# Kernel optimization log

Measured on AMD Instinct MI355X. Metric: run time of the kernel, lower is better.

Reference implementation:

```python
import jax, jax.numpy as jnp
import numpy as np

N, IN_DIM, E, EDGE_DIM = 50000, 128, 600000, 16
D, H, L = 128, 4, 2
C = D // H  # 32
NEG_SLOPE = 0.2
EPS = 1e-5


def setup_inputs() -> dict:
    key = jax.random.key(0)
    ks = jax.random.split(key, 20)
    x = jax.random.normal(ks[0], (N, IN_DIM), dtype=jnp.float32)
    src = jax.random.randint(ks[1], (E,), 0, N)
    dst = jax.random.randint(ks[2], (E,), 0, N)
    src = jnp.where(src == dst, (src + 1) % N, src)  # no pre-existing self loops
    edge_index = jnp.stack([src, dst]).astype(jnp.int64)
    edge_attr = jax.random.normal(ks[3], (E, EDGE_DIM), dtype=jnp.float32)
    s = 0.05
    p = {
        'in_w': jax.random.normal(ks[4], (IN_DIM, D)) * s,
        'in_b': jnp.zeros((D,), jnp.float32),
        'Wl': jax.random.normal(ks[5], (L, D, D)) * s,
        'bl': jnp.zeros((L, D), jnp.float32),
        'Wr': jax.random.normal(ks[6], (L, D, D)) * s,
        'br': jnp.zeros((L, D), jnp.float32),
        'We': jax.random.normal(ks[7], (L, EDGE_DIM, D)) * s,
        'att': jax.random.normal(ks[8], (L, H, C)) * s,
        'cb': jnp.zeros((L, D), jnp.float32),
        'ln_g': jnp.ones((D,), jnp.float32),
        'ln_b': jnp.zeros((D,), jnp.float32),
        'h1w': jax.random.normal(ks[9], (D, D // 2)) * s,
        'h1b': jnp.zeros((D // 2,), jnp.float32),
        'h2w': jax.random.normal(ks[10], (D // 2, 3)) * s,
        'h2b': jnp.zeros((3,), jnp.float32),
    }
    return {'x': x, 'edge_index': edge_index, 'edge_attr': edge_attr, **p}


def _forward(x, edge_attr, in_w, in_b, Wl, bl, Wr, br, We, att, cb,
             ln_g, ln_b, h1w, h1b, h2w, h2b, src0, dst0):
    n = x.shape[0]
    # add_self_loops with fill_value='mean': loop edge_attr = mean of incoming edge_attr per node
    deg = jax.ops.segment_sum(jnp.ones_like(dst0, dtype=x.dtype), dst0, n)
    loop_attr = jax.ops.segment_sum(edge_attr, dst0, n) / jnp.maximum(deg, 1.0)[:, None]
    idx = jnp.arange(n, dtype=src0.dtype)
    src = jnp.concatenate([src0, idx])
    dst = jnp.concatenate([dst0, idx])
    ea = jnp.concatenate([edge_attr, loop_attr])  # [E+N, EDGE_DIM]

    h = x @ in_w + in_b  # [N, D]
    for l in range(L):
        xl = (h @ Wl[l] + bl[l]).reshape(n, H, C)
        xr = (h @ Wr[l] + br[l]).reshape(n, H, C)
        ee = (ea @ We[l]).reshape(-1, H, C)
        m = xl[src] + xr[dst] + ee                      # [E', H, C]
        m = jnp.where(m > 0, m, NEG_SLOPE * m)          # LeakyReLU(0.2)
        logit = jnp.einsum('ehc,hc->eh', m, att[l])     # [E', H]
        mx = jax.ops.segment_max(logit, dst, n)         # every node has a self loop -> finite
        a = jnp.exp(logit - mx[dst])
        den = jax.ops.segment_sum(a, dst, n)
        a = a / den[dst]                                # scatter softmax over destinations
        out = jax.ops.segment_sum(a[..., None] * xl[src], dst, n)  # [N, H, C]
        h = jax.nn.elu(out.reshape(n, D) + cb[l])       # conv bias then ELU (dropout=eval)
    mu = jnp.mean(h, axis=-1, keepdims=True)
    var = jnp.mean((h - mu) ** 2, axis=-1, keepdims=True)
    h = (h - mu) * jax.lax.rsqrt(var + EPS) * ln_g + ln_b
    h = jax.nn.relu(h @ h1w + h1b)
    return h @ h2w + h2b  # [N, 3]


def reference(x, edge_index, edge_attr, in_w, in_b, Wl, bl, Wr, br, We, att, cb,
              ln_g, ln_b, h1w, h1b, h2w, h2b):
    return _forward(x, edge_attr, in_w, in_b, Wl, bl, Wr, br, We, att, cb,
                    ln_g, ln_b, h1w, h1b, h2w, h2b, edge_index[0], edge_index[1])
```

## Files before the change

### kernel.cpp

```cpp
#include <hip/hip_runtime.h>

#define NEG_SLOPE 0.2f
#define LN_EPS 1e-5f

typedef float f2 __attribute__((ext_vector_type(2)));
typedef short s16x4 __attribute__((ext_vector_type(4)));
typedef short s16x8 __attribute__((ext_vector_type(8)));
typedef float f32x4 __attribute__((ext_vector_type(4)));
typedef unsigned au32 __attribute__((may_alias));

__device__ __forceinline__ f2 sp2(float x){ return (f2){x, x}; }
__device__ __forceinline__ f2 fma2(f2 a, f2 b, f2 c){
#if __has_builtin(__builtin_elementwise_fma)
  return __builtin_elementwise_fma(a, b, c);
#else
  f2 r; r.x = fmaf(a.x, b.x, c.x); r.y = fmaf(a.y, b.y, c.y); return r;
#endif
}
__device__ __forceinline__ f2 max2(f2 a, f2 b){
#if __has_builtin(__builtin_elementwise_max)
  return __builtin_elementwise_max(a, b);
#else
  f2 r; r.x = fmaxf(a.x, b.x); r.y = fmaxf(a.y, b.y); return r;
#endif
}
__device__ __forceinline__ f2 min2(f2 a, f2 b){
#if __has_builtin(__builtin_elementwise_min)
  return __builtin_elementwise_min(a, b);
#else
  f2 r; r.x = fminf(a.x, b.x); r.y = fminf(a.y, b.y); return r;
#endif
}
__device__ __forceinline__ float wsum64(float v){
  #pragma unroll
  for (int o = 32; o >= 1; o >>= 1) v += __shfl_xor(v, o);
  return v;
}
__device__ __forceinline__ unsigned short f2b(float f){
  unsigned u = __float_as_uint(f);
  return (unsigned short)((u + 0x7fffu + ((u >> 16) & 1u)) >> 16);
}

__global__ void k_count(const int* __restrict__ dst, int* __restrict__ deg, int E){
  int e = blockIdx.x * blockDim.x + threadIdx.x;
  if (e < E) atomicAdd(&deg[dst[e]], 1);
}

__global__ void k_scan_blk(const int* __restrict__ deg, int* __restrict__ part,
                           int* __restrict__ sums, int n){
  __shared__ int buf[256];
  int t = threadIdx.x, i = blockIdx.x * 256 + t;
  int v = (i < n) ? deg[i] : 0;
  buf[t] = v; __syncthreads();
  #pragma unroll
  for (int off = 1; off < 256; off <<= 1){
    int x = (t >= off) ? buf[t - off] : 0;
    __syncthreads(); buf[t] += x; __syncthreads();
  }
  if (i < n) part[i] = buf[t] - v;
  if (t == 255) sums[blockIdx.x] = buf[255];
}

__global__ void k_scan_top(int* __restrict__ sums, int nb){
  __shared__ int buf[256];
  int t = threadIdx.x;
  int v = (t < nb) ? sums[t] : 0;
  buf[t] = v; __syncthreads();
  #pragma unroll
  for (int off = 1; off < 256; off <<= 1){
    int x = (t >= off) ? buf[t - off] : 0;
    __syncthreads(); buf[t] += x; __syncthreads();
  }
  if (t < nb) sums[t] = buf[t] - v;
}

__global__ void k_scan_add(int* __restrict__ ptr, const int* __restrict__ sums,
                           int n, int Etot){
  int i = blockIdx.x * 256 + threadIdx.x;
  if (i < n) ptr[i] += sums[blockIdx.x];
  if (i == 0) ptr[n] = Etot;
}

__global__ void k_fill(const int* __restrict__ dst, const int* __restrict__ src,
                       int* __restrict__ cnt, const int* __restrict__ ptr,
                       const float* __restrict__ ea, unsigned short* __restrict__ ceab,
                       int* __restrict__ sx, int E){
  int e = blockIdx.x * blockDim.x + threadIdx.x;
  if (e < E){
    int d = dst[e];
    int pos = atomicAdd(&cnt[d], 1);
    int p = ptr[d] + pos;
    sx[p] = src[e];
    const float4* s4 = (const float4*)(ea + (size_t)e * 16);
    float4 a0 = s4[0], a1 = s4[1], a2 = s4[2], a3 = s4[3];
    ushort4 o0 = {f2b(a0.x), f2b(a0.y), f2b(a0.z), f2b(a0.w)};
    ushort4 o1 = {f2b(a1.x), f2b(a1.y), f2b(a1.z), f2b(a1.w)};
    ushort4 o2 = {f2b(a2.x), f2b(a2.y), f2b(a2.z), f2b(a2.w)};
    ushort4 o3 = {f2b(a3.x), f2b(a3.y), f2b(a3.z), f2b(a3.w)};
    ushort4* d4 = (ushort4*)(ceab + (size_t)p * 16);
    d4[0] = o0; d4[1] = o1; d4[2] = o2; d4[3] = o3;
  }
}

__global__ void k_cvt(const float* __restrict__ X, unsigned short* __restrict__ Xb,
                      long n4){
  long i = (long)blockIdx.x * blockDim.x + threadIdx.x;
  long i4 = i * 4;
  if (i4 < n4){
    float4 v = *(const float4*)(X + i4);
    ushort4 o; o.x = f2b(v.x); o.y = f2b(v.y); o.z = f2b(v.z); o.w = f2b(v.w);
    *(ushort4*)(Xb + i4) = o;
  }
}

__global__ void k_pack(const float* __restrict__ w0, const float* __restrict__ w1,
                       const float* __restrict__ w2, const float* __restrict__ w3,
                       const float* __restrict__ w4, unsigned short* __restrict__ Bp){
  int id = blockIdx.x * blockDim.x + threadIdx.x;
  if (id >= 5 * 2048) return;
  int mat = id >> 11, rem = id & 2047;
  int c = rem >> 8, q = (rem >> 6) & 3, l = rem & 63;
  const float* W = mat == 0 ? w0 : mat == 1 ? w1 : mat == 2 ? w2 : mat == 3 ? w3 : w4;
  unsigned short* o = Bp + ((size_t)mat * 2048 + rem) * 8;
  int kb = q * 32 + (l >> 4) * 8;
  int col = c * 16 + (l & 15);
  #pragma unroll
  for (int j = 0; j < 8; j++) o[j] = f2b(W[(kb + j) * 128 + col]);
}

__global__ void k_packwe(const float* __restrict__ We, unsigned short* __restrict__ Bpwe){
  int id = blockIdx.x * blockDim.x + threadIdx.x;
  if (id >= 2 * 8 * 64) return;
  int layer = id >> 9, rem = id & 511, c = rem >> 6, l = rem & 63;
  const float* W = We + (size_t)layer * 2048;
  unsigned short* o = Bpwe + (size_t)id * 8;
  int kb = (l >> 4) * 8;
  int col = c * 16 + (l & 15);
  #pragma unroll
  for (int j = 0; j < 8; j++){
    int k = kb + j;
    o[j] = (k < 16) ? f2b(W[k * 128 + col]) : (unsigned short)0;
  }
}

__launch_bounds__(256)
__global__ void k_mm(const unsigned short* __restrict__ A,
                     const unsigned short* __restrict__ Bp,
                     const float* __restrict__ bias,
                     unsigned short* __restrict__ Yb, int M){
  const int ln = threadIdx.x & 63;
  const int rowBase = (blockIdx.x * 4 + (threadIdx.x >> 6)) * 16;
  const int r16 = ln & 15, quad = ln >> 4;
  int row = rowBase + r16; if (row >= M) row = M - 1;
  const unsigned short* ap = A + (size_t)row * 128 + quad * 8;
  s16x8 af[4];
  #pragma unroll
  for (int q = 0; q < 4; q++) af[q] = *(const s16x8*)(ap + q * 32);
  f32x4 acc[8];
  #pragma unroll
  for (int c = 0; c < 8; c++){
    acc[c] = (f32x4){0.f, 0.f, 0.f, 0.f};
    #pragma unroll
    for (int q = 0; q < 4; q++){
      s16x8 bf = *(const s16x8*)(Bp + ((size_t)(c * 4 + q) * 64 + ln) * 8);
      acc[c] = __builtin_amdgcn_mfma_f32_16x16x32_bf16(af[q], bf, acc[c], 0, 0, 0);
    }
  }
  #pragma unroll
  for (int c = 0; c < 8; c++){
    int col = c * 16 + r16;
    float bv = bias[col];
    #pragma unroll
    for (int r = 0; r < 4; r++){
      int orow = rowBase + quad * 4 + r;
      if (orow < M) Yb[(size_t)orow * 128 + col] = f2b(acc[c][r] + bv);
    }
  }
}

__launch_bounds__(256)
__global__ void k_mm_lr(const unsigned short* __restrict__ A,
                        const unsigned short* __restrict__ BpL,
                        const unsigned short* __restrict__ BpR,
                        const float* __restrict__ bL, const float* __restrict__ bR,
                        float* __restrict__ YL, float* __restrict__ YR, int M){
  const int ln = threadIdx.x & 63;
  const int rowBase = (blockIdx.x * 4 + (threadIdx.x >> 6)) * 16;
  const int r16 = ln & 15, quad = ln >> 4;
  int row = rowBase + r16; if (row >= M) row = M - 1;
  const unsigned short* ap = A + (size_t)row * 128 + quad * 8;
  s16x8 af[4];
  #pragma unroll
  for (int q = 0; q < 4; q++) af[q] = *(const s16x8*)(ap + q * 32);
  f32x4 aL[8], aR[8];
  #pragma unroll
  for (int c = 0; c < 8; c++){
    aL[c] = (f32x4){0.f, 0.f, 0.f, 0.f};
    aR[c] = (f32x4){0.f, 0.f, 0.f, 0.f};
    #pragma unroll
    for (int q = 0; q < 4; q++){
      s16x8 bfl = *(const s16x8*)(BpL + ((size_t)(c * 4 + q) * 64 + ln) * 8);
      s16x8 bfr = *(const s16x8*)(BpR + ((size_t)(c * 4 + q) * 64 + ln) * 8);
      aL[c] = __builtin_amdgcn_mfma_f32_16x16x32_bf16(af[q], bfl, aL[c], 0, 0, 0);
      aR[c] = __builtin_amdgcn_mfma_f32_16x16x32_bf16(af[q], bfr, aR[c], 0, 0, 0);
    }
  }
  #pragma unroll
  for (int c = 0; c < 8; c++){
    int col = c * 16 + r16;
    float bvl = bL[col], bvr = bR[col];
    #pragma unroll
    for (int r = 0; r < 4; r++){
      int orow = rowBase + quad * 4 + r;
      if (orow < M){
        YL[(size_t)orow * 128 + col] = aL[c][r] + bvl;
        YR[(size_t)orow * 128 + col] = aR[c][r] + bvr;
      }
    }
  }
}

__launch_bounds__(256)
__global__ void k_gat(const float* __restrict__ xl, const float* __restrict__ xr,
                      const unsigned short* __restrict__ ceab,
                      const int* __restrict__ sx, const int* __restrict__ ptr,
                      const unsigned short* __restrict__ Bpwe,
                      const float* __restrict__ att, const float* __restrict__ cbv,
                      float* __restrict__ hf, unsigned short* __restrict__ hb,
                      int N, int wf, int wb){
  __shared__ unsigned short lee[4][16 * 130];
  const int t = threadIdx.x & 63;
  const int wv = threadIdx.x >> 6;
  const int c0 = 2 * t;
  const int l15 = t & 15, q = t >> 4;

  s16x8 bwe[8];
  #pragma unroll
  for (int c = 0; c < 8; c++) bwe[c] = *(const s16x8*)(Bpwe + ((size_t)c * 64 + t) * 8);
  const f2 atv = *(const f2*)(att + c0);
  const f2 cbf = *(const f2*)(cbv + c0);
  unsigned short* lw = &lee[wv][0];
  const int wbase = q * 4 * 130 + l15;

  for (int n = blockIdx.x * 4 + wv; n < N; n += gridDim.x * 4){
    const int beg = __builtin_amdgcn_readfirstlane(ptr[n]);
    const int end = __builtin_amdgcn_readfirstlane(ptr[n + 1]);
    const int deg = end - beg;

    const f2 xrv = *(const f2*)(xr + (size_t)n * 128 + c0);
    const f2 xln = *(const f2*)(xl + (size_t)n * 128 + c0);

    f2 acc = sp2(0.f), eesum = sp2(0.f);
    float den = 0.f;

    for (int cbase = beg; cbase < end; cbase += 64){
      const int cn = __builtin_amdgcn_readfirstlane(min(64, end - cbase));
      int sv = (t < cn) ? sx[cbase + t] : 0;

      for (int sub = 0; sub < cn; sub += 16){
        s16x8 af = (s16x8){0, 0, 0, 0, 0, 0, 0, 0};
        if (q < 2)
          af = *(const s16x8*)(ceab + (size_t)(cbase + sub + l15) * 16 + q * 8);
        f2 xs[16];
        #pragma unroll
        for (int i = 0; i < 16; i++){
          int s = __builtin_amdgcn_readlane(sv, sub + i);
          xs[i] = *(const f2*)(xl + (size_t)s * 128 + c0);
        }
        #pragma unroll
        for (int c = 0; c < 8; c++){
          f32x4 ee4 = __builtin_amdgcn_mfma_f32_16x16x32_bf16(
              af, bwe[c], (f32x4){0.f, 0.f, 0.f, 0.f}, 0, 0, 0);
          #pragma unroll
          for (int r = 0; r < 4; r++)
            lw[wbase + r * 130 + c * 16] = f2b(ee4[r]);
        }
        #pragma unroll
        for (int i = 0; i < 16; i++){
          const int item = sub + i;
          const float vm = (item < cn) ? 1.f : 0.f;
          const int it = (item < cn) ? i : 0;
          au32 pp = *(const au32*)&lw[it * 130 + c0];
          f2 ee;
          ee.x = __uint_as_float(pp << 16);
          ee.y = __uint_as_float(pp & 0xffff0000u);
          eesum = fma2(sp2(vm), ee, eesum);
          f2 m = xs[i] + xrv + ee;
          m = fma2(sp2(NEG_SLOPE), min2(m, sp2(0.f)), max2(m, sp2(0.f)));
          f2 pr = m * atv;
          float pl = pr.x + pr.y;
          pl += __shfl_xor(pl, 1); pl += __shfl_xor(pl, 2);
          pl += __shfl_xor(pl, 4); pl += __shfl_xor(pl, 8);
          float p = __expf(pl) * vm;
          den += p;
          acc = fma2(sp2(p), xs[i], acc);
        }
      }
    }

    {
      float rdeg = 1.f / fmaxf((float)deg, 1.f);
      f2 m = xln + xrv + eesum * sp2(rdeg);
      m = fma2(sp2(NEG_SLOPE), min2(m, sp2(0.f)), max2(m, sp2(0.f)));
      f2 pr = m * atv;
      float pl = pr.x + pr.y;
      pl += __shfl_xor(pl, 1); pl += __shfl_xor(pl, 2);
      pl += __shfl_xor(pl, 4); pl += __shfl_xor(pl, 8);
      float p = __expf(pl);
      den += p;
      acc = fma2(sp2(p), xln, acc);
    }

    float rd = 1.f / den;
    f2 o = fma2(acc, sp2(rd), cbf);
    float o0 = o.x > 0.f ? o.x : expm1f(o.x);
    float o1 = o.y > 0.f ? o.y : expm1f(o.y);
    if (wf) *(f2*)(hf + (size_t)n * 128 + c0) = (f2){o0, o1};
    if (wb){
      unsigned packed = (unsigned)f2b(o0) | ((unsigned)f2b(o1) << 16);
      *(unsigned*)(hb + (size_t)n * 128 + c0) = packed;
    }
  }
}

__launch_bounds__(256)
__global__ void k_head(const float* __restrict__ h, const float* __restrict__ g,
                       const float* __restrict__ b, const float* __restrict__ w1,
                       const float* __restrict__ b1, const float* __restrict__ w2,
                       const float* __restrict__ b2, float* __restrict__ out, int N){
  __shared__ float sn[4][128];
  const int t = threadIdx.x & 63, wv = threadIdx.x >> 6;
  for (int node = blockIdx.x * 4 + wv; node < N; node += gridDim.x * 4){
    float h0 = h[(size_t)node * 128 + t];
    float h1 = h[(size_t)node * 128 + 64 + t];
    float mu = wsum64(h0 + h1) * (1.f / 128.f);
    float d0 = h0 - mu, d1 = h1 - mu;
    float var = wsum64(d0 * d0 + d1 * d1) * (1.f / 128.f);
    float rstd = rsqrtf(var + LN_EPS);
    sn[wv][t]      = d0 * rstd * g[t]      + b[t];
    sn[wv][t + 64] = d1 * rstd * g[t + 64] + b[t + 64];
    float a = b1[t];
    #pragma unroll
    for (int k4 = 0; k4 < 32; k4++){
      float4 v = *(const float4*)&sn[wv][k4 * 4];
      a = fmaf(v.x, w1[(k4 * 4 + 0) * 64 + t], a);
      a = fmaf(v.y, w1[(k4 * 4 + 1) * 64 + t], a);
      a = fmaf(v.z, w1[(k4 * 4 + 2) * 64 + t], a);
      a = fmaf(v.w, w1[(k4 * 4 + 3) * 64 + t], a);
    }
    a = fmaxf(a, 0.f);
    float p0 = a * w2[t * 3 + 0], p1 = a * w2[t * 3 + 1], p2 = a * w2[t * 3 + 2];
    p0 = wsum64(p0); p1 = wsum64(p1); p2 = wsum64(p2);
    if (t == 0){
      out[(size_t)node * 3 + 0] = p0 + b2[0];
      out[(size_t)node * 3 + 1] = p1 + b2[1];
      out[(size_t)node * 3 + 2] = p2 + b2[2];
    }
  }
}

extern "C" void kernel_launch(void* const* d_in, const int* in_sizes, int n_in,
                              void* d_out, int out_size, void* d_ws, size_t ws_size,
                              hipStream_t stream){
  const float* x    = (const float*)d_in[0];
  const int*   ei   = (const int*)d_in[1];
  const float* ea   = (const float*)d_in[2];
  const float* in_w = (const float*)d_in[3];
  const float* in_b = (const float*)d_in[4];
  const float* Wl   = (const float*)d_in[5];
  const float* bl   = (const float*)d_in[6];
  const float* Wr   = (const float*)d_in[7];
  const float* br   = (const float*)d_in[8];
  const float* We   = (const float*)d_in[9];
  const float* att  = (const float*)d_in[10];
  const float* cb   = (const float*)d_in[11];
  const float* lng  = (const float*)d_in[12];
  const float* lnb  = (const float*)d_in[13];
  const float* h1w  = (const float*)d_in[14];
  const float* h1b  = (const float*)d_in[15];
  const float* h2w  = (const float*)d_in[16];
  const float* h2b  = (const float*)d_in[17];
  float* out = (float*)d_out;

  int N = in_sizes[0] / 128;
  int E = in_sizes[1] / 2;
  const int* src = ei;
  const int* dst = ei + E;

  char* w = (char*)d_ws;
  size_t off = 0;
  auto alloc = [&](size_t bytes) -> char* {
    char* p = w + off;
    off = (off + bytes + 255) & ~(size_t)255;
    return p;
  };
  int*   deg   = (int*)alloc((size_t)N * 4);
  int*   cnt   = (int*)alloc((size_t)N * 4);
  int*   ptr   = (int*)alloc((size_t)(N + 1) * 4);
  int*   bsum  = (int*)alloc(256 * 4);
  int*   sx    = (int*)alloc((size_t)E * 4);
  unsigned short* ceab = (unsigned short*)alloc((size_t)(E + 64) * 16 * 2);
  unsigned short* xb    = (unsigned short*)alloc((size_t)N * 128 * 2);
  unsigned short* hb_in = (unsigned short*)alloc((size_t)N * 128 * 2);
  unsigned short* Bp    = (unsigned short*)alloc((size_t)5 * 16384 * 2);
  unsigned short* Bpwe  = (unsigned short*)alloc((size_t)2 * 4096 * 2);
  float* hf    = (float*)alloc((size_t)N * 128 * 4);
  float* xlb   = (float*)alloc((size_t)N * 128 * 4);
  float* xrb   = (float*)alloc((size_t)N * 128 * 4);

  int nb = (N + 255) / 256;
  hipMemsetAsync(deg, 0, (size_t)N * 4, stream);
  hipMemsetAsync(cnt, 0, (size_t)N * 4, stream);
  k_count<<<(E + 255) / 256, 256, 0, stream>>>(dst, deg, E);
  k_scan_blk<<<nb, 256, 0, stream>>>(deg, ptr, bsum, N);
  k_scan_top<<<1, 256, 0, stream>>>(bsum, nb);
  k_scan_add<<<nb, 256, 0, stream>>>(ptr, bsum, N, E);
  k_fill<<<(E + 255) / 256, 256, 0, stream>>>(dst, src, cnt, ptr, ea, ceab, sx, E);

  long n4 = (long)N * 128;
  k_cvt<<<(int)((n4 / 4 + 255) / 256), 256, 0, stream>>>(x, xb, n4);
  k_pack<<<(5 * 2048 + 255) / 256, 256, 0, stream>>>(in_w, Wl, Wl + 16384, Wr, Wr + 16384, Bp);
  k_packwe<<<4, 256, 0, stream>>>(We, Bpwe);

  int gblocks = (N + 63) / 64;
  int nodeBlocks = (N + 3) / 4;
  int gatBlocks = nodeBlocks < 2048 ? nodeBlocks : 2048;
  k_mm<<<gblocks, 256, 0, stream>>>(xb, Bp, in_b, hb_in, N);
  for (int l = 0; l < 2; l++){
    const unsigned short* Ain = (l == 0) ? hb_in : xb;
    k_mm_lr<<<gblocks, 256, 0, stream>>>(Ain, Bp + (size_t)(1 + l) * 16384,
                                         Bp + (size_t)(3 + l) * 16384,
                                         bl + l * 128, br + l * 128, xlb, xrb, N);
    k_gat<<<gatBlocks, 256, 0, stream>>>(xlb, xrb, ceab, sx, ptr,
                                         Bpwe + (size_t)l * 4096,
                                         att + l * 128, cb + l * 128,
                                         hf, xb, N, (l == 1) ? 1 : 0, (l == 0) ? 1 : 0);
  }
  k_head<<<gatBlocks, 256, 0, stream>>>(hf, lng, lnb, h1w, h1b, h2w, h2b, out, N);
}
```

Baseline: 486.4 us.

## Fold input projection into layer-0 weights, store xl/xr as bf16, merge prep kernels

```diff
diff --git a/kernel.cpp b/kernel.cpp
--- a/kernel.cpp
+++ b/kernel.cpp
@@ -4,7 +4,6 @@
 #define LN_EPS 1e-5f
 
 typedef float f2 __attribute__((ext_vector_type(2)));
-typedef short s16x4 __attribute__((ext_vector_type(4)));
 typedef short s16x8 __attribute__((ext_vector_type(8)));
 typedef float f32x4 __attribute__((ext_vector_type(4)));
 typedef unsigned au32 __attribute__((may_alias));
@@ -39,6 +38,12 @@
 __device__ __forceinline__ unsigned short f2b(float f){
   unsigned u = __float_as_uint(f);
   return (unsigned short)((u + 0x7fffu + ((u >> 16) & 1u)) >> 16);
+}
+__device__ __forceinline__ f2 b2f2(unsigned pp){
+  f2 r;
+  r.x = __uint_as_float(pp << 16);
+  r.y = __uint_as_float(pp & 0xffff0000u);
+  return r;
 }
 
 __global__ void k_count(const int* __restrict__ dst, int* __restrict__ deg, int E){
@@ -102,78 +107,73 @@
   }
 }
 
-__global__ void k_cvt(const float* __restrict__ X, unsigned short* __restrict__ Xb,
-                      long n4){
-  long i = (long)blockIdx.x * blockDim.x + threadIdx.x;
-  long i4 = i * 4;
-  if (i4 < n4){
-    float4 v = *(const float4*)(X + i4);
+__global__ void k_fold(const float* __restrict__ in_w, const float* __restrict__ in_b,
+                       const float* __restrict__ Wl0, const float* __restrict__ bl0,
+                       const float* __restrict__ Wr0, const float* __restrict__ br0,
+                       float* __restrict__ Wcl, float* __restrict__ bcl,
+                       float* __restrict__ Wcr, float* __restrict__ bcr){
+  int id = blockIdx.x * blockDim.x + threadIdx.x;
+  if (id < 2 * 16384){
+    int m = id >> 14, rem = id & 16383;
+    int k = rem >> 7, c = rem & 127;
+    const float* W = m ? Wr0 : Wl0;
+    float s = 0.f;
+    #pragma unroll 4
+    for (int d = 0; d < 128; d++) s = fmaf(in_w[k * 128 + d], W[d * 128 + c], s);
+    (m ? Wcr : Wcl)[k * 128 + c] = s;
+  } else if (id < 2 * 16384 + 256){
+    int id2 = id - 2 * 16384;
+    int m = id2 >> 7, c = id2 & 127;
+    const float* W = m ? Wr0 : Wl0;
+    float s = (m ? br0 : bl0)[c];
+    for (int d = 0; d < 128; d++) s = fmaf(in_b[d], W[d * 128 + c], s);
+    (m ? bcr : bcl)[c] = s;
+  }
+}
+
+__global__ void k_prep(const float* __restrict__ x, const float* __restrict__ Wcl,
+                       const float* __restrict__ Wl1, const float* __restrict__ Wcr,
+                       const float* __restrict__ Wr1, const float* __restrict__ We,
+                       unsigned short* __restrict__ xb, int* __restrict__ deg,
+                       int* __restrict__ cnt, unsigned short* __restrict__ Bp,
+                       unsigned short* __restrict__ Bpwe, int N, long n4){
+  long id = (long)blockIdx.x * blockDim.x + threadIdx.x;
+  long nc4 = n4 / 4;
+  if (id < nc4){
+    long i4 = id * 4;
+    float4 v = *(const float4*)(x + i4);
     ushort4 o; o.x = f2b(v.x); o.y = f2b(v.y); o.z = f2b(v.z); o.w = f2b(v.w);
-    *(ushort4*)(Xb + i4) = o;
-  }
-}
-
-__global__ void k_pack(const float* __restrict__ w0, const float* __restrict__ w1,
-                       const float* __restrict__ w2, const float* __restrict__ w3,
-                       const float* __restrict__ w4, unsigned short* __restrict__ Bp){
-  int id = blockIdx.x * blockDim.x + threadIdx.x;
-  if (id >= 5 * 2048) return;
-  int mat = id >> 11, rem = id & 2047;
-  int c = rem >> 8, q = (rem >> 6) & 3, l = rem & 63;
-  const float* W = mat == 0 ? w0 : mat == 1 ? w1 : mat == 2 ? w2 : mat == 3 ? w3 : w4;
-  unsigned short* o = Bp + ((size_t)mat * 2048 + rem) * 8;
-  int kb = q * 32 + (l >> 4) * 8;
-  int col = c * 16 + (l & 15);
-  #pragma unroll
-  for (int j = 0; j < 8; j++) o[j] = f2b(W[(kb + j) * 128 + col]);
-}
-
-__global__ void k_packwe(const float* __restrict__ We, unsigned short* __restrict__ Bpwe){
-  int id = blockIdx.x * blockDim.x + threadIdx.x;
-  if (id >= 2 * 8 * 64) return;
-  int layer = id >> 9, rem = id & 511, c = rem >> 6, l = rem & 63;
-  const float* W = We + (size_t)layer * 2048;
-  unsigned short* o = Bpwe + (size_t)id * 8;
-  int kb = (l >> 4) * 8;
-  int col = c * 16 + (l & 15);
-  #pragma unroll
-  for (int j = 0; j < 8; j++){
-    int k = kb + j;
-    o[j] = (k < 16) ? f2b(W[k * 128 + col]) : (unsigned short)0;
-  }
-}
-
-__launch_bounds__(256)
-__global__ void k_mm(const unsigned short* __restrict__ A,
-                     const unsigned short* __restrict__ Bp,
-                     const float* __restrict__ bias,
-                     unsigned short* __restrict__ Yb, int M){
-  const int ln = threadIdx.x & 63;
-  const int rowBase = (blockIdx.x * 4 + (threadIdx.x >> 6)) * 16;
-  const int r16 = ln & 15, quad = ln >> 4;
-  int row = rowBase + r16; if (row >= M) row = M - 1;
-  const unsigned short* ap = A + (size_t)row * 128 + quad * 8;
-  s16x8 af[4];
-  #pragma unroll
-  for (int q = 0; q < 4; q++) af[q] = *(const s16x8*)(ap + q * 32);
-  f32x4 acc[8];
-  #pragma unroll
-  for (int c = 0; c < 8; c++){
-    acc[c] = (f32x4){0.f, 0.f, 0.f, 0.f};
+    *(ushort4*)(xb + i4) = o;
+    return;
+  }
+  id -= nc4;
+  if (id < 2 * (long)N){
+    if (id < N) deg[id] = 0; else cnt[id - N] = 0;
+    return;
+  }
+  id -= 2 * (long)N;
+  if (id < 4 * 2048){
+    int mat = (int)(id >> 11), rem = (int)(id & 2047);
+    int c = rem >> 8, q = (rem >> 6) & 3, l = rem & 63;
+    const float* W = mat == 0 ? Wcl : mat == 1 ? Wl1 : mat == 2 ? Wcr : Wr1;
+    unsigned short* o = Bp + ((size_t)mat * 2048 + rem) * 8;
+    int kb = q * 32 + (l >> 4) * 8;
+    int col = c * 16 + (l & 15);
     #pragma unroll
-    for (int q = 0; q < 4; q++){
-      s16x8 bf = *(const s16x8*)(Bp + ((size_t)(c * 4 + q) * 64 + ln) * 8);
-      acc[c] = __builtin_amdgcn_mfma_f32_16x16x32_bf16(af[q], bf, acc[c], 0, 0, 0);
-    }
-  }
-  #pragma unroll
-  for (int c = 0; c < 8; c++){
-    int col = c * 16 + r16;
-    float bv = bias[col];
+    for (int j = 0; j < 8; j++) o[j] = f2b(W[(kb + j) * 128 + col]);
+    return;
+  }
+  id -= 4 * 2048;
+  if (id < 2 * 8 * 64){
+    int layer = (int)(id >> 9), rem = (int)(id & 511), c = rem >> 6, l = rem & 63;
+    const float* W = We + (size_t)layer * 2048;
+    unsigned short* o = Bpwe + (size_t)id * 8;
+    int kb = (l >> 4) * 8;
+    int col = c * 16 + (l & 15);
     #pragma unroll
-    for (int r = 0; r < 4; r++){
-      int orow = rowBase + quad * 4 + r;
-      if (orow < M) Yb[(size_t)orow * 128 + col] = f2b(acc[c][r] + bv);
+    for (int j = 0; j < 8; j++){
+      int k = kb + j;
+      o[j] = (k < 16) ? f2b(W[k * 128 + col]) : (unsigned short)0;
     }
   }
 }
@@ -183,7 +183,8 @@
                         const unsigned short* __restrict__ BpL,
                         const unsigned short* __restrict__ BpR,
                         const float* __restrict__ bL, const float* __restrict__ bR,
-                        float* __restrict__ YL, float* __restrict__ YR, int M){
+                        unsigned short* __restrict__ YL, unsigned short* __restrict__ YR,
+                        int M){
   const int ln = threadIdx.x & 63;
   const int rowBase = (blockIdx.x * 4 + (threadIdx.x >> 6)) * 16;
   const int r16 = ln & 15, quad = ln >> 4;
@@ -213,15 +214,16 @@
     for (int r = 0; r < 4; r++){
       int orow = rowBase + quad * 4 + r;
       if (orow < M){
-        YL[(size_t)orow * 128 + col] = aL[c][r] + bvl;
-        YR[(size_t)orow * 128 + col] = aR[c][r] + bvr;
+        YL[(size_t)orow * 128 + col] = f2b(aL[c][r] + bvl);
+        YR[(size_t)orow * 128 + col] = f2b(aR[c][r] + bvr);
       }
     }
   }
 }
 
 __launch_bounds__(256)
-__global__ void k_gat(const float* __restrict__ xl, const float* __restrict__ xr,
+__global__ void k_gat(const unsigned short* __restrict__ xl,
+                      const unsigned short* __restrict__ xr,
                       const unsigned short* __restrict__ ceab,
                       const int* __restrict__ sx, const int* __restrict__ ptr,
                       const unsigned short* __restrict__ Bpwe,
@@ -233,6 +235,7 @@
   const int wv = threadIdx.x >> 6;
   const int c0 = 2 * t;
   const int l15 = t & 15, q = t >> 4;
+  const int stride = gridDim.x * 4;
 
   s16x8 bwe[8];
   #pragma unroll
@@ -242,13 +245,20 @@
   unsigned short* lw = &lee[wv][0];
   const int wbase = q * 4 * 130 + l15;
 
-  for (int n = blockIdx.x * 4 + wv; n < N; n += gridDim.x * 4){
-    const int beg = __builtin_amdgcn_readfirstlane(ptr[n]);
-    const int end = __builtin_amdgcn_readfirstlane(ptr[n + 1]);
+  int n = blockIdx.x * 4 + wv;
+  int pb = 0, pe = 0;
+  if (n < N){ pb = ptr[n]; pe = ptr[n + 1]; }
+  while (n < N){
+    int nn = n + stride;
+    int pb2 = 0, pe2 = 0;
+    if (nn < N){ pb2 = ptr[nn]; pe2 = ptr[nn + 1]; }
+
+    const int beg = __builtin_amdgcn_readfirstlane(pb);
+    const int end = __builtin_amdgcn_readfirstlane(pe);
     const int deg = end - beg;
 
-    const f2 xrv = *(const f2*)(xr + (size_t)n * 128 + c0);
-    const f2 xln = *(const f2*)(xl + (size_t)n * 128 + c0);
+    const f2 xrv = b2f2(*(const au32*)(xr + (size_t)n * 128 + c0));
+    const f2 xln = b2f2(*(const au32*)(xl + (size_t)n * 128 + c0));
 
     f2 acc = sp2(0.f), eesum = sp2(0.f);
     float den = 0.f;
@@ -261,11 +271,11 @@
         s16x8 af = (s16x8){0, 0, 0, 0, 0, 0, 0, 0};
         if (q < 2)
           af = *(const s16x8*)(ceab + (size_t)(cbase + sub + l15) * 16 + q * 8);
-        f2 xs[16];
+        au32 xs[16];
         #pragma unroll
         for (int i = 0; i < 16; i++){
           int s = __builtin_amdgcn_readlane(sv, sub + i);
-          xs[i] = *(const f2*)(xl + (size_t)s * 128 + c0);
+          xs[i] = *(const au32*)(xl + (size_t)s * 128 + c0);
         }
         #pragma unroll
         for (int c = 0; c < 8; c++){
@@ -281,11 +291,10 @@
           const float vm = (item < cn) ? 1.f : 0.f;
           const int it = (item < cn) ? i : 0;
           au32 pp = *(const au32*)&lw[it * 130 + c0];
-          f2 ee;
-          ee.x = __uint_as_float(pp << 16);
-          ee.y = __uint_as_float(pp & 0xffff0000u);
+          f2 ee = b2f2(pp);
+          f2 xv = b2f2(xs[i]);
           eesum = fma2(sp2(vm), ee, eesum);
-          f2 m = xs[i] + xrv + ee;
+          f2 m = xv + xrv + ee;
           m = fma2(sp2(NEG_SLOPE), min2(m, sp2(0.f)), max2(m, sp2(0.f)));
           f2 pr = m * atv;
           float pl = pr.x + pr.y;
@@ -293,7 +302,7 @@
           pl += __shfl_xor(pl, 4); pl += __shfl_xor(pl, 8);
           float p = __expf(pl) * vm;
           den += p;
-          acc = fma2(sp2(p), xs[i], acc);
+          acc = fma2(sp2(p), xv, acc);
         }
       }
     }
@@ -320,6 +329,8 @@
       unsigned packed = (unsigned)f2b(o0) | ((unsigned)f2b(o1) << 16);
       *(unsigned*)(hb + (size_t)n * 128 + c0) = packed;
     }
+
+    n = nn; pb = pb2; pe = pe2;
   }
 }
 
@@ -400,41 +411,47 @@
   int*   bsum  = (int*)alloc(256 * 4);
   int*   sx    = (int*)alloc((size_t)E * 4);
   unsigned short* ceab = (unsigned short*)alloc((size_t)(E + 64) * 16 * 2);
-  unsigned short* xb    = (unsigned short*)alloc((size_t)N * 128 * 2);
-  unsigned short* hb_in = (unsigned short*)alloc((size_t)N * 128 * 2);
-  unsigned short* Bp    = (unsigned short*)alloc((size_t)5 * 16384 * 2);
-  unsigned short* Bpwe  = (unsigned short*)alloc((size_t)2 * 4096 * 2);
-  float* hf    = (float*)alloc((size_t)N * 128 * 4);
-  float* xlb   = (float*)alloc((size_t)N * 128 * 4);
-  float* xrb   = (float*)alloc((size_t)N * 128 * 4);
+  unsigned short* xb   = (unsigned short*)alloc((size_t)N * 128 * 2);
+  unsigned short* g0   = (unsigned short*)alloc((size_t)N * 128 * 2);
+  unsigned short* Bp   = (unsigned short*)alloc((size_t)4 * 16384 * 2);
+  unsigned short* Bpwe = (unsigned short*)alloc((size_t)2 * 4096 * 2);
+  float* Wcl  = (float*)alloc((size_t)16384 * 4);
+  float* Wcr  = (float*)alloc((size_t)16384 * 4);
+  float* bcl  = (float*)alloc(128 * 4);
+  float* bcr  = (float*)alloc(128 * 4);
+  float* hf   = (float*)alloc((size_t)N * 128 * 4);
+  unsigned short* xlb = (unsigned short*)alloc((size_t)N * 128 * 2);
+  unsigned short* xrb = (unsigned short*)alloc((size_t)N * 128 * 2);
+
+  k_fold<<<(2 * 16384 + 256 + 255) / 256, 256, 0, stream>>>(
+      in_w, in_b, Wl, bl, Wr, br, Wcl, bcl, Wcr, bcr);
+
+  long n4 = (long)N * 128;
+  long total = n4 / 4 + 2 * (long)N + 4 * 2048 + 2 * 8 * 64;
+  k_prep<<<(int)((total + 255) / 256), 256, 0, stream>>>(
+      x, Wcl, Wl + 16384, Wcr, Wr + 16384, We, xb, deg, cnt, Bp, Bpwe, N, n4);
 
   int nb = (N + 255) / 256;
-  hipMemsetAsync(deg, 0, (size_t)N * 4, stream);
-  hipMemsetAsync(cnt, 0, (size_t)N * 4, stream);
   k_count<<<(E + 255) / 256, 256, 0, stream>>>(dst, deg, E);
   k_scan_blk<<<nb, 256, 0, stream>>>(deg, ptr, bsum, N);
   k_scan_top<<<1, 256, 0, stream>>>(bsum, nb);
   k_scan_add<<<nb, 256, 0, stream>>>(ptr, bsum, N, E);
   k_fill<<<(E + 255) / 256, 256, 0, stream>>>(dst, src, cnt, ptr, ea, ceab, sx, E);
 
-  long n4 = (long)N * 128;
-  k_cvt<<<(int)((n4 / 4 + 255) / 256), 256, 0, stream>>>(x, xb, n4);
-  k_pack<<<(5 * 2048 + 255) / 256, 256, 0, stream>>>(in_w, Wl, Wl + 16384, Wr, Wr + 16384, Bp);
-  k_packwe<<<4, 256, 0, stream>>>(We, Bpwe);
-
   int gblocks = (N + 63) / 64;
   int nodeBlocks = (N + 3) / 4;
   int gatBlocks = nodeBlocks < 2048 ? nodeBlocks : 2048;
-  k_mm<<<gblocks, 256, 0, stream>>>(xb, Bp, in_b, hb_in, N);
   for (int l = 0; l < 2; l++){
-    const unsigned short* Ain = (l == 0) ? hb_in : xb;
-    k_mm_lr<<<gblocks, 256, 0, stream>>>(Ain, Bp + (size_t)(1 + l) * 16384,
-                                         Bp + (size_t)(3 + l) * 16384,
-                                         bl + l * 128, br + l * 128, xlb, xrb, N);
+    const unsigned short* Ain = (l == 0) ? xb : g0;
+    const float* bLp = (l == 0) ? bcl : bl + 128;
+    const float* bRp = (l == 0) ? bcr : br + 128;
+    k_mm_lr<<<gblocks, 256, 0, stream>>>(Ain, Bp + (size_t)l * 16384,
+                                         Bp + (size_t)(2 + l) * 16384,
+                                         bLp, bRp, xlb, xrb, N);
     k_gat<<<gatBlocks, 256, 0, stream>>>(xlb, xrb, ceab, sx, ptr,
                                          Bpwe + (size_t)l * 4096,
                                          att + l * 128, cb + l * 128,
-                                         hf, xb, N, (l == 1) ? 1 : 0, (l == 0) ? 1 : 0);
+                                         hf, g0, N, (l == 1) ? 1 : 0, (l == 0) ? 1 : 0);
   }
   k_head<<<gatBlocks, 256, 0, stream>>>(hf, lng, lnb, h1w, h1b, h2w, h2b, out, N);
 }
```

New measurement: 471.3 us. -3.1%, faster.
